# Kernel tuning notes

Measured on AMD Instinct MI355X. Metric: run time of the kernel, lower is better.

The kernel has to match this reference:

```python
import jax, jax.numpy as jnp
import numpy as np

# Config (matches init_kwargs)
B, DIM = 16, 768
HEADS, DHEAD = 12, 64
H_MEM, W_MEM = 16, 16           # memory grid; N = 256 tokens
MAX_AH, MAX_AW = 3, 3
N = H_MEM * W_MEM


def _area_pool(t):
    """t: [B', N, D] laid out on an H_MEM x W_MEM grid.
    Returns (area_sums [B', M, D], area_sizes [M]) over all rectangle sizes
    (ah, aw) with 1<=ah<=MAX_AH, 1<=aw<=MAX_AW, at every valid position,
    via a 2D integral image (summed-area table)."""
    Bp, _, D = t.shape
    g = t.reshape(Bp, H_MEM, W_MEM, D)
    I = jnp.cumsum(jnp.cumsum(g, axis=1), axis=2)
    I = jnp.pad(I, ((0, 0), (1, 0), (1, 0), (0, 0)))  # [B', H+1, W+1, D]
    sums, sizes = [], []
    for ah in range(1, MAX_AH + 1):
        for aw in range(1, MAX_AW + 1):
            s = (I[:, ah:, aw:] - I[:, :-ah, aw:]
                 - I[:, ah:, :-aw] + I[:, :-ah, :-aw])  # [B', H-ah+1, W-aw+1, D]
            n_pos = s.shape[1] * s.shape[2]
            sums.append(s.reshape(Bp, n_pos, D))
            sizes.append(np.full((n_pos,), float(ah * aw), dtype=np.float32))
    return jnp.concatenate(sums, axis=1), jnp.asarray(np.concatenate(sizes))


def setup_inputs() -> dict:
    key = jax.random.key(0)
    ks = jax.random.split(key, 10)
    s = 0.02
    d = dict(
        x=jax.random.normal(ks[0], (B, N, DIM), jnp.float32),
        # to_qkv: Linear(dim, 3*dim, bias=False); stored as (in, out)
        w_qkv=jax.random.normal(ks[1], (DIM, 3 * DIM), jnp.float32) * s,
        # per-head q/k/v projections (dim -> heads*dim_head) with bias
        w_q=jax.random.normal(ks[2], (DIM, HEADS * DHEAD), jnp.float32) * s,
        b_q=jnp.zeros((HEADS * DHEAD,), jnp.float32),
        w_k=jax.random.normal(ks[3], (DIM, HEADS * DHEAD), jnp.float32) * s,
        b_k=jnp.zeros((HEADS * DHEAD,), jnp.float32),
        w_v=jax.random.normal(ks[4], (DIM, HEADS * DHEAD), jnp.float32) * s,
        b_v=jnp.zeros((HEADS * DHEAD,), jnp.float32),
        # output projection (heads*dim_head -> dim)
        w_o=jax.random.normal(ks[5], (HEADS * DHEAD, DIM), jnp.float32) * s,
        b_o=jnp.zeros((DIM,), jnp.float32),
    )
    return d


def reference(x, w_qkv, w_q, b_q, w_k, b_k, w_v, b_v, w_o, b_o):
    # QKV projection + split: 'b n (qkv d) -> qkv b n d'
    qkv = x @ w_qkv                               # [B, N, 3*DIM]
    q, k, v = jnp.split(qkv, 3, axis=-1)          # each [B, N, DIM]

    def to_heads(t, w, b):                        # 'b n (h d) -> (b h) n d'
        return ((t @ w + b)
                .reshape(B, N, HEADS, DHEAD)
                .transpose(0, 2, 1, 3)
                .reshape(B * HEADS, N, DHEAD))

    qh = to_heads(q, w_q, b_q)
    kh = to_heads(k, w_k, b_k)
    vh = to_heads(v, w_v, b_v)

    # Area keys: mean over each area; area values: sum over each area.
    k_sum, sizes = _area_pool(kh)                 # [BH, M, d], [M]
    k_area = k_sum / sizes[None, :, None]
    v_area, _ = _area_pool(vh)                    # [BH, M, d]

    logits = jnp.einsum('bqd,bmd->bqm', qh, k_area)   # [BH, N, M]
    weights = jax.nn.softmax(logits, axis=-1)
    out = jnp.einsum('bqm,bmd->bqd', weights, v_area)  # [BH, N, d]

    # '(b h) n d -> b n (h d)' then output projection
    out = (out.reshape(B, HEADS, N, DHEAD)
              .transpose(0, 2, 1, 3)
              .reshape(B, N, HEADS * DHEAD))
    return out @ w_o + b_o
```

## Files before the change

### kernel.cpp

```cpp
#include <hip/hip_runtime.h>
#include <hip/hip_bf16.h>

typedef __hip_bfloat16 bf16;
typedef __attribute__((ext_vector_type(8))) short short8b;
typedef __attribute__((ext_vector_type(4))) short short4b;
typedef __attribute__((ext_vector_type(4))) float f32x4;

#define NAREA 2025
#define NAREA_PAD 2048

static __device__ __forceinline__ float b2f(bf16 x) { return __bfloat162float(x); }
static __device__ __forceinline__ short f2bs(float f) {
  bf16 h = __float2bfloat16(f);
  return *(short*)&h;
}

__global__ __launch_bounds__(256) void k_cast(
    const float* __restrict__ x, const float* __restrict__ wqkv,
    bf16* __restrict__ xb, bf16* __restrict__ wqkvb)
{
  int idx = (blockIdx.x * 256 + threadIdx.x) * 4;
  const int NX = 4096 * 768;
  float4 v;
  bf16* d;
  if (idx < NX) { v = *(const float4*)(x + idx); d = xb + idx; }
  else { v = *(const float4*)(wqkv + (idx - NX)); d = wqkvb + (idx - NX); }
  short4b s = {f2bs(v.x), f2bs(v.y), f2bs(v.z), f2bs(v.w)};
  *(short4b*)d = s;
}

__global__ __launch_bounds__(256) void k_tcast(
    const float* __restrict__ s0, const float* __restrict__ s1,
    const float* __restrict__ s2, bf16* __restrict__ d0,
    bf16* __restrict__ d1, bf16* __restrict__ d2)
{
  __shared__ float tile[32][33];
  int z = blockIdx.z;
  const float* src = (z == 0) ? s0 : (z == 1) ? s1 : s2;
  bf16* dst = (z == 0) ? d0 : (z == 1) ? d1 : d2;
  int r0 = blockIdx.y * 32, c0 = blockIdx.x * 32;
  int lx = threadIdx.x & 31, ly = threadIdx.x >> 5;
#pragma unroll
  for (int yy = 0; yy < 4; ++yy)
    tile[ly + yy * 8][lx] = src[(size_t)(r0 + ly + yy * 8) * 768 + c0 + lx];
  __syncthreads();
#pragma unroll
  for (int yy = 0; yy < 4; ++yy)
    dst[(size_t)(c0 + ly + yy * 8) * 768 + r0 + lx] =
        __float2bfloat16(tile[lx][ly + yy * 8]);
}


__global__ __launch_bounds__(256) void k_combine_m(
    const bf16* __restrict__ wqkvb, const bf16* __restrict__ wqT,
    const bf16* __restrict__ wkT, const bf16* __restrict__ wvT,
    bf16* __restrict__ WcTb)
{
  __shared__ __align__(16) short As[2][128 * 32];
  __shared__ __align__(16) short Bs[2][128 * 32];
  const int t3 = blockIdx.z;
  const bf16* BT = (t3 == 0) ? wqT : (t3 == 1) ? wkT : wvT;
  const int m0 = blockIdx.y * 128, n0 = blockIdx.x * 128;
  const int tid = threadIdx.x, lane = tid & 63, w = tid >> 6;
  const int tt = lane & 15, q4 = lane >> 4;
  const int moff = (w & 1) * 64, noff = (w >> 1) * 64;
  const int r_a = tid >> 2, kc = (tid & 3) * 8;

  f32x4 acc[4][4];
#pragma unroll
  for (int i = 0; i < 4; ++i)
#pragma unroll
    for (int j = 0; j < 4; ++j) acc[i][j] = (f32x4){0.f, 0.f, 0.f, 0.f};

  uint4 ra0 = *(const uint4*)(wqkvb + (size_t)(m0 + r_a) * 2304 + t3 * 768 + kc);
  uint4 ra1 = *(const uint4*)(wqkvb + (size_t)(m0 + r_a + 64) * 2304 + t3 * 768 + kc);
  uint4 rb0 = *(const uint4*)(BT + (size_t)(n0 + r_a) * 768 + kc);
  uint4 rb1 = *(const uint4*)(BT + (size_t)(n0 + r_a + 64) * 768 + kc);

  for (int it = 0; it < 24; ++it) {
    short* as = As[it & 1];
    short* bs = Bs[it & 1];
    *(uint4*)&as[r_a * 32 + kc] = ra0;
    *(uint4*)&as[(r_a + 64) * 32 + kc] = ra1;
    *(uint4*)&bs[r_a * 32 + kc] = rb0;
    *(uint4*)&bs[(r_a + 64) * 32 + kc] = rb1;
    if (it < 23) {
      int k0 = (it + 1) * 32;
      ra0 = *(const uint4*)(wqkvb + (size_t)(m0 + r_a) * 2304 + t3 * 768 + k0 + kc);
      ra1 = *(const uint4*)(wqkvb + (size_t)(m0 + r_a + 64) * 2304 + t3 * 768 + k0 + kc);
      rb0 = *(const uint4*)(BT + (size_t)(n0 + r_a) * 768 + k0 + kc);
      rb1 = *(const uint4*)(BT + (size_t)(n0 + r_a + 64) * 768 + k0 + kc);
    }
    __syncthreads();
    short8b afr[4], bfr[4];
#pragma unroll
    for (int mt = 0; mt < 4; ++mt)
      afr[mt] = *(const short8b*)&as[(moff + mt * 16 + tt) * 32 + q4 * 8];
#pragma unroll
    for (int nt = 0; nt < 4; ++nt)
      bfr[nt] = *(const short8b*)&bs[(noff + nt * 16 + tt) * 32 + q4 * 8];
#pragma unroll
    for (int mt = 0; mt < 4; ++mt)
#pragma unroll
      for (int nt = 0; nt < 4; ++nt)
        acc[mt][nt] = __builtin_amdgcn_mfma_f32_16x16x32_bf16(afr[mt], bfr[nt], acc[mt][nt], 0, 0, 0);
  }

  bf16* C = WcTb + (size_t)t3 * 768 * 768;
#pragma unroll
  for (int nt = 0; nt < 4; ++nt) {
    int n = n0 + noff + nt * 16 + tt;
#pragma unroll
    for (int mt = 0; mt < 4; ++mt) {
      int mb = m0 + moff + mt * 16 + q4 * 4;
      short4b v = {f2bs(acc[mt][nt][0]), f2bs(acc[mt][nt][1]),
                   f2bs(acc[mt][nt][2]), f2bs(acc[mt][nt][3])};
      *(short4b*)&C[(size_t)n * 768 + mb] = v;
    }
  }
}

__global__ __launch_bounds__(256) void k_proj_m(
    const bf16* __restrict__ xb, const bf16* __restrict__ WcTb,
    const float* __restrict__ bq, const float* __restrict__ bk,
    const float* __restrict__ bv,
    bf16* __restrict__ qh, bf16* __restrict__ kh, bf16* __restrict__ vh)
{
  __shared__ __align__(16) short As[2][128 * 32];
  __shared__ __align__(16) short Bs[2][128 * 32];
  const int t3 = blockIdx.z;
  const bf16* BT = WcTb + (size_t)t3 * 768 * 768;
  const float* bias = (t3 == 0) ? bq : (t3 == 1) ? bk : bv;
  bf16* dst = (t3 == 0) ? qh : (t3 == 1) ? kh : vh;
  const int m0 = blockIdx.y * 128, n0 = blockIdx.x * 128;
  const int tid = threadIdx.x, lane = tid & 63, w = tid >> 6;
  const int tt = lane & 15, q4 = lane >> 4;
  const int moff = (w & 1) * 64, noff = (w >> 1) * 64;
  const int r_a = tid >> 2, kc = (tid & 3) * 8;

  f32x4 acc[4][4];
#pragma unroll
  for (int i = 0; i < 4; ++i)
#pragma unroll
    for (int j = 0; j < 4; ++j) acc[i][j] = (f32x4){0.f, 0.f, 0.f, 0.f};

  uint4 ra0 = *(const uint4*)(xb + (size_t)(m0 + r_a) * 768 + kc);
  uint4 ra1 = *(const uint4*)(xb + (size_t)(m0 + r_a + 64) * 768 + kc);
  uint4 rb0 = *(const uint4*)(BT + (size_t)(n0 + r_a) * 768 + kc);
  uint4 rb1 = *(const uint4*)(BT + (size_t)(n0 + r_a + 64) * 768 + kc);

  for (int it = 0; it < 24; ++it) {
    short* as = As[it & 1];
    short* bs = Bs[it & 1];
    *(uint4*)&as[r_a * 32 + kc] = ra0;
    *(uint4*)&as[(r_a + 64) * 32 + kc] = ra1;
    *(uint4*)&bs[r_a * 32 + kc] = rb0;
    *(uint4*)&bs[(r_a + 64) * 32 + kc] = rb1;
    if (it < 23) {
      int k0 = (it + 1) * 32;
      ra0 = *(const uint4*)(xb + (size_t)(m0 + r_a) * 768 + k0 + kc);
      ra1 = *(const uint4*)(xb + (size_t)(m0 + r_a + 64) * 768 + k0 + kc);
      rb0 = *(const uint4*)(BT + (size_t)(n0 + r_a) * 768 + k0 + kc);
      rb1 = *(const uint4*)(BT + (size_t)(n0 + r_a + 64) * 768 + k0 + kc);
    }
    __syncthreads();
    short8b afr[4], bfr[4];
#pragma unroll
    for (int mt = 0; mt < 4; ++mt)
      afr[mt] = *(const short8b*)&as[(moff + mt * 16 + tt) * 32 + q4 * 8];
#pragma unroll
    for (int nt = 0; nt < 4; ++nt)
      bfr[nt] = *(const short8b*)&bs[(noff + nt * 16 + tt) * 32 + q4 * 8];
#pragma unroll
    for (int mt = 0; mt < 4; ++mt)
#pragma unroll
      for (int nt = 0; nt < 4; ++nt)
        acc[mt][nt] = __builtin_amdgcn_mfma_f32_16x16x32_bf16(afr[mt], bfr[nt], acc[mt][nt], 0, 0, 0);
  }

#pragma unroll
  for (int nt = 0; nt < 4; ++nt) {
    int c = n0 + noff + nt * 16 + tt;
    float bv = bias[c];
    int h = c >> 6, d = c & 63;
#pragma unroll
    for (int mt = 0; mt < 4; ++mt) {
#pragma unroll
      for (int r = 0; r < 4; ++r) {
        int m = m0 + moff + mt * 16 + q4 * 4 + r;
        dst[(((size_t)((m >> 8) * 12 + h)) << 14) + ((m & 255) << 6) + d] =
            __float2bfloat16(acc[mt][nt][r] + bv);
      }
    }
  }
}

__global__ __launch_bounds__(256) void k_out_m(
    const bf16* __restrict__ attno, const bf16* __restrict__ woT,
    const float* __restrict__ bo, float* __restrict__ out)
{
  __shared__ __align__(16) short As[2][128 * 32];
  __shared__ __align__(16) short Bs[2][128 * 32];
  const int m0 = blockIdx.y * 128, n0 = blockIdx.x * 128;
  const int tid = threadIdx.x, lane = tid & 63, w = tid >> 6;
  const int tt = lane & 15, q4 = lane >> 4;
  const int moff = (w & 1) * 64, noff = (w >> 1) * 64;
  const int r_a = tid >> 2, kc = (tid & 3) * 8;

  f32x4 acc[4][4];
#pragma unroll
  for (int i = 0; i < 4; ++i)
#pragma unroll
    for (int j = 0; j < 4; ++j) acc[i][j] = (f32x4){0.f, 0.f, 0.f, 0.f};

  int m_a0 = m0 + r_a, m_a1 = m0 + r_a + 64;
  uint4 ra0 = *(const uint4*)(attno + (((size_t)((m_a0 >> 8) * 12 + (kc >> 6))) << 14) + ((m_a0 & 255) << 6) + (kc & 63));
  uint4 ra1 = *(const uint4*)(attno + (((size_t)((m_a1 >> 8) * 12 + (kc >> 6))) << 14) + ((m_a1 & 255) << 6) + (kc & 63));
  uint4 rb0 = *(const uint4*)(woT + (size_t)(n0 + r_a) * 768 + kc);
  uint4 rb1 = *(const uint4*)(woT + (size_t)(n0 + r_a + 64) * 768 + kc);

  for (int it = 0; it < 24; ++it) {
    short* as = As[it & 1];
    short* bs = Bs[it & 1];
    *(uint4*)&as[r_a * 32 + kc] = ra0;
    *(uint4*)&as[(r_a + 64) * 32 + kc] = ra1;
    *(uint4*)&bs[r_a * 32 + kc] = rb0;
    *(uint4*)&bs[(r_a + 64) * 32 + kc] = rb1;
    if (it < 23) {
      int k = (it + 1) * 32 + kc;
      ra0 = *(const uint4*)(attno + (((size_t)((m_a0 >> 8) * 12 + (k >> 6))) << 14) + ((m_a0 & 255) << 6) + (k & 63));
      ra1 = *(const uint4*)(attno + (((size_t)((m_a1 >> 8) * 12 + (k >> 6))) << 14) + ((m_a1 & 255) << 6) + (k & 63));
      rb0 = *(const uint4*)(woT + (size_t)(n0 + r_a) * 768 + k);
      rb1 = *(const uint4*)(woT + (size_t)(n0 + r_a + 64) * 768 + k);
    }
    __syncthreads();
    short8b afr[4], bfr[4];
#pragma unroll
    for (int mt = 0; mt < 4; ++mt)
      afr[mt] = *(const short8b*)&as[(moff + mt * 16 + tt) * 32 + q4 * 8];
#pragma unroll
    for (int nt = 0; nt < 4; ++nt)
      bfr[nt] = *(const short8b*)&bs[(noff + nt * 16 + tt) * 32 + q4 * 8];
#pragma unroll
    for (int mt = 0; mt < 4; ++mt)
#pragma unroll
      for (int nt = 0; nt < 4; ++nt)
        acc[mt][nt] = __builtin_amdgcn_mfma_f32_16x16x32_bf16(afr[mt], bfr[nt], acc[mt][nt], 0, 0, 0);
  }

#pragma unroll
  for (int nt = 0; nt < 4; ++nt) {
    int c = n0 + noff + nt * 16 + tt;
    float bv = bo[c];
#pragma unroll
    for (int mt = 0; mt < 4; ++mt)
#pragma unroll
      for (int r = 0; r < 4; ++r) {
        int m = m0 + moff + mt * 16 + q4 * 4 + r;
        out[(size_t)m * 768 + c] = acc[mt][nt][r] + bv;
      }
  }
}

__global__ __launch_bounds__(256) void k_rect(int4* __restrict__ rectG,
                                              float* __restrict__ invG)
{
  int m = blockIdx.x * 256 + threadIdx.x;
  if (m >= NAREA_PAD) return;
  int4 rc = make_int4(0, 0, 0, 0);
  float iv = 0.f;
  if (m < NAREA) {
    int rem = m, ah = 1, aw = 1, found = 0;
    for (int a = 1; a <= 3 && !found; ++a)
      for (int w = 1; w <= 3 && !found; ++w) {
        int np = (17 - a) * (17 - w);
        if (rem < np) { ah = a; aw = w; found = 1; }
        else rem -= np;
      }
    int cw = 17 - aw;
    int y = rem / cw, x = rem - y * cw;
    rc.x = (y * 17 + x) * 64;
    rc.y = (y * 17 + (x + aw)) * 64;
    rc.z = ((y + ah) * 17 + x) * 64;
    rc.w = ((y + ah) * 17 + (x + aw)) * 64;
    iv = 1.0f / (float)(ah * aw);
  }
  rectG[m] = rc;
  invG[m] = iv;
}

__global__ __launch_bounds__(128) void k_integral(
    const bf16* __restrict__ kh, const bf16* __restrict__ vh,
    float* __restrict__ Ik, float* __restrict__ Iv)
{
  int bh = blockIdx.x;
  int d = threadIdx.x & 63;
  bool isv = threadIdx.x >= 64;
  const bf16* src = (isv ? vh : kh) + ((size_t)bh << 14);
  float* dst = (isv ? Iv : Ik) + (size_t)bh * 18496;
  float prev[17];
#pragma unroll
  for (int i = 0; i < 17; ++i) prev[i] = 0.f;
#pragma unroll
  for (int xx = 0; xx < 17; ++xx) dst[xx * 64 + d] = 0.f;
#pragma unroll 1
  for (int y = 1; y <= 16; ++y) {
    dst[(y * 17) * 64 + d] = 0.f;
    float rs = 0.f;
#pragma unroll
    for (int xx = 1; xx <= 16; ++xx) {
      rs += b2f(src[((y - 1) * 16 + (xx - 1)) * 64 + d]);
      float cur = prev[xx] + rs;
      dst[(y * 17 + xx) * 64 + d] = cur;
      prev[xx] = cur;
    }
  }
}

__global__ __launch_bounds__(1024) void k_attn_m(
    const bf16* __restrict__ qh, const float* __restrict__ Ik,
    const float* __restrict__ Iv, const int4* __restrict__ rectG,
    const float* __restrict__ invG, bf16* __restrict__ attno)
{
  __shared__ __align__(16) short aK2[2][64 * 72];
  __shared__ __align__(16) short aVt2[2][64 * 72];
  __shared__ __align__(16) short Pb[16][16 * 72];

  const int tid = threadIdx.x;
  const int lane = tid & 63;
  const int w = tid >> 6;
  const int t = lane & 15;
  const int q4 = lane >> 4;
  const int bh = blockIdx.x;

  const float* Ikb = Ik + (size_t)bh * 18496;
  const float* Ivb = Iv + (size_t)bh * 18496;
  const bf16* qbase = qh + ((size_t)bh << 14);

  short8b qf0 = *(const short8b*)(qbase + (w * 16 + t) * 64 + q4 * 8);
  short8b qf1 = *(const short8b*)(qbase + (w * 16 + t) * 64 + 32 + q4 * 8);

  f32x4 O[4];
#pragma unroll
  for (int i = 0; i < 4; ++i) O[i] = (f32x4){0.f, 0.f, 0.f, 0.f};
  float l = 0.f;

  {
    short* aK = aK2[0];
    short* aVt = aVt2[0];
#pragma unroll
    for (int i = 0; i < 4; ++i) {
      int j = w * 4 + i;
      int4 rc = rectG[j];
      float iv = invG[j];
      float kc = Ikb[rc.w + lane] - Ikb[rc.y + lane] - Ikb[rc.z + lane] + Ikb[rc.x + lane];
      float vc = Ivb[rc.w + lane] - Ivb[rc.y + lane] - Ivb[rc.z + lane] + Ivb[rc.x + lane];
      aK[j * 72 + lane] = f2bs(kc * iv);
      aVt[lane * 72 + j] = f2bs(vc);
    }
  }

  for (int it = 0; it < 32; ++it) {
    __syncthreads();
    const short* aK = aK2[it & 1];
    const short* aVt = aVt2[it & 1];
    if (it + 1 < 32) {
      int t0n = (it + 1) * 64;
      short* aKn = aK2[(it + 1) & 1];
      short* aVtn = aVt2[(it + 1) & 1];
#pragma unroll
      for (int i = 0; i < 4; ++i) {
        int j = w * 4 + i;
        int4 rc = rectG[t0n + j];
        float iv = invG[t0n + j];
        float kc = Ikb[rc.w + lane] - Ikb[rc.y + lane] - Ikb[rc.z + lane] + Ikb[rc.x + lane];
        float vc = Ivb[rc.w + lane] - Ivb[rc.y + lane] - Ivb[rc.z + lane] + Ivb[rc.x + lane];
        aKn[j * 72 + lane] = f2bs(kc * iv);
        aVtn[lane * 72 + j] = f2bs(vc);
      }
    }

    const int t0 = it * 64;
    const bool edge = (t0 + 64 > NAREA);
#pragma unroll
    for (int at = 0; at < 4; ++at) {
      short8b af0 = *(const short8b*)&aK[(at * 16 + t) * 72 + q4 * 8];
      short8b af1 = *(const short8b*)&aK[(at * 16 + t) * 72 + 32 + q4 * 8];
      f32x4 s = (f32x4){0.f, 0.f, 0.f, 0.f};
      s = __builtin_amdgcn_mfma_f32_16x16x32_bf16(af0, qf0, s, 0, 0, 0);
      s = __builtin_amdgcn_mfma_f32_16x16x32_bf16(af1, qf1, s, 0, 0, 0);
      float p[4];
#pragma unroll
      for (int r = 0; r < 4; ++r) {
        p[r] = __expf(s[r]);
        if (edge && (t0 + at * 16 + q4 * 4 + r >= NAREA)) p[r] = 0.f;
      }
      l += (p[0] + p[1]) + (p[2] + p[3]);
      short4b pk = (short4b){f2bs(p[0]), f2bs(p[1]), f2bs(p[2]), f2bs(p[3])};
      *(short4b*)&Pb[w][t * 72 + at * 16 + q4 * 4] = pk;
    }
    short8b pf0 = *(const short8b*)&Pb[w][t * 72 + q4 * 8];
    short8b pf1 = *(const short8b*)&Pb[w][t * 72 + 32 + q4 * 8];
#pragma unroll
    for (int nt = 0; nt < 4; ++nt) {
      short8b vf0 = *(const short8b*)&aVt[(nt * 16 + t) * 72 + q4 * 8];
      short8b vf1 = *(const short8b*)&aVt[(nt * 16 + t) * 72 + 32 + q4 * 8];
      O[nt] = __builtin_amdgcn_mfma_f32_16x16x32_bf16(pf0, vf0, O[nt], 0, 0, 0);
      O[nt] = __builtin_amdgcn_mfma_f32_16x16x32_bf16(pf1, vf1, O[nt], 0, 0, 0);
    }
  }

  l += __shfl_xor(l, 16, 64);
  l += __shfl_xor(l, 32, 64);

  bf16* ob = attno + ((size_t)bh << 14);
#pragma unroll
  for (int r = 0; r < 4; ++r) {
    int qrow = q4 * 4 + r;
    float invl = 1.0f / __shfl(l, qrow, 64);
#pragma unroll
    for (int nt = 0; nt < 4; ++nt)
      ob[(w * 16 + qrow) * 64 + nt * 16 + t] = __float2bfloat16(O[nt][r] * invl);
  }
}

extern "C" void kernel_launch(void* const* d_in, const int* in_sizes, int n_in,
                              void* d_out, int out_size, void* d_ws, size_t ws_size,
                              hipStream_t stream) {
  const float* x    = (const float*)d_in[0];
  const float* wqkv = (const float*)d_in[1];
  const float* wq   = (const float*)d_in[2];
  const float* bq   = (const float*)d_in[3];
  const float* wk   = (const float*)d_in[4];
  const float* bk   = (const float*)d_in[5];
  const float* wv   = (const float*)d_in[6];
  const float* bv   = (const float*)d_in[7];
  const float* wo   = (const float*)d_in[8];
  const float* bo   = (const float*)d_in[9];
  float* out = (float*)d_out;

  char* ws = (char*)d_ws;
  char* ob = (char*)d_out;
  const size_t WC_B = 7077888;
  const size_t QH_B = 6291456;

  bf16* xb    = (bf16*)ob;
  bf16* WcTb  = (bf16*)(ob + QH_B);
  bf16* attno = (bf16*)ws;
  int4*  rectG = (int4*)(ws + QH_B);
  float* invG  = (float*)(ws + QH_B + 32768);
  bf16* qh = (bf16*)(ws + WC_B);
  bf16* kh = (bf16*)(ws + WC_B + QH_B);
  bf16* vh = (bf16*)(ws + WC_B + 2 * QH_B);
  bf16* wqkvb = (bf16*)(ws + WC_B);
  bf16* wqT   = (bf16*)(ws + WC_B + 3538944);
  bf16* wkT   = (bf16*)(ws + WC_B + 4718592);
  bf16* wvT   = (bf16*)(ws + WC_B + 5898240);
  float* Ik = (float*)(ws + WC_B + 3 * QH_B);
  float* Iv = Ik + 3551232;
  bf16* woT = (bf16*)(ws + WC_B + 3 * QH_B);

  k_cast<<<dim3(4800), 256, 0, stream>>>(x, wqkv, xb, wqkvb);
  k_tcast<<<dim3(24, 24, 3), 256, 0, stream>>>(wq, wk, wv, wqT, wkT, wvT);
  k_combine_m<<<dim3(6, 6, 3), 256, 0, stream>>>(wqkvb, wqT, wkT, wvT, WcTb);
  k_proj_m<<<dim3(6, 32, 3), 256, 0, stream>>>(xb, WcTb, bq, bk, bv, qh, kh, vh);
  k_rect<<<dim3(8), 256, 0, stream>>>(rectG, invG);
  k_integral<<<dim3(192), 128, 0, stream>>>(kh, vh, Ik, Iv);
  k_attn_m<<<dim3(192), 1024, 0, stream>>>(qh, Ik, Iv, rectG, invG, attno);
  k_tcast<<<dim3(24, 24, 1), 256, 0, stream>>>(wo, wo, wo, woT, woT, woT);
  k_out_m<<<dim3(6, 32), 256, 0, stream>>>(attno, woT, bo, out);
}
```

Baseline: 256.0 us.

## Split attention over area chunks across four blocks and merge partials

The area-attention kernel now splits the 2025-area loop into four chunks per (batch, head), so the grid grows from 192 to 768 blocks. The old grid left many CUs idle. Each split writes an unnormalised partial output and a partial softmax denominator to scratch buffers that reuse dead workspace and output memory. A new merge kernel sums the partials and normalises. The transposed V stores into shared memory are also packed into one 4-short vector write. The cost is an extra kernel launch and extra global traffic for the partials. Storing the partials and denominators in bf16 also loses some precision.

New measurement: 293.1 us. 14.5% more time.

```diff
diff --git a/kernel.cpp b/kernel.cpp
--- a/kernel.cpp
+++ b/kernel.cpp
@@ -13,6 +13,9 @@
 static __device__ __forceinline__ short f2bs(float f) {
   bf16 h = __float2bfloat16(f);
   return *(short*)&h;
+}
+static __device__ __forceinline__ float s2f(short s) {
+  return __uint_as_float(((unsigned)(unsigned short)s) << 16);
 }
 
 __global__ __launch_bounds__(256) void k_cast(
@@ -181,7 +184,7 @@
 #pragma unroll
   for (int nt = 0; nt < 4; ++nt) {
     int c = n0 + noff + nt * 16 + tt;
-    float bv = bias[c];
+    float bvv = bias[c];
     int h = c >> 6, d = c & 63;
 #pragma unroll
     for (int mt = 0; mt < 4; ++mt) {
@@ -189,7 +192,7 @@
       for (int r = 0; r < 4; ++r) {
         int m = m0 + moff + mt * 16 + q4 * 4 + r;
         dst[(((size_t)((m >> 8) * 12 + h)) << 14) + ((m & 255) << 6) + d] =
-            __float2bfloat16(acc[mt][nt][r] + bv);
+            __float2bfloat16(acc[mt][nt][r] + bvv);
       }
     }
   }
@@ -251,13 +254,13 @@
 #pragma unroll
   for (int nt = 0; nt < 4; ++nt) {
     int c = n0 + noff + nt * 16 + tt;
-    float bv = bo[c];
+    float bvv = bo[c];
 #pragma unroll
     for (int mt = 0; mt < 4; ++mt)
 #pragma unroll
       for (int r = 0; r < 4; ++r) {
         int m = m0 + moff + mt * 16 + q4 * 4 + r;
-        out[(size_t)m * 768 + c] = acc[mt][nt][r] + bv;
+        out[(size_t)m * 768 + c] = acc[mt][nt][r] + bvv;
       }
   }
 }
@@ -317,10 +320,11 @@
   }
 }
 
-__global__ __launch_bounds__(1024) void k_attn_m(
+__global__ __launch_bounds__(1024, 8) void k_attn_m(
     const bf16* __restrict__ qh, const float* __restrict__ Ik,
     const float* __restrict__ Iv, const int4* __restrict__ rectG,
-    const float* __restrict__ invG, bf16* __restrict__ attno)
+    const float* __restrict__ invG, bf16* __restrict__ opA,
+    bf16* __restrict__ opB, bf16* __restrict__ lp)
 {
   __shared__ __align__(16) short aK2[2][64 * 72];
   __shared__ __align__(16) short aVt2[2][64 * 72];
@@ -331,7 +335,9 @@
   const int w = tid >> 6;
   const int t = lane & 15;
   const int q4 = lane >> 4;
-  const int bh = blockIdx.x;
+  const int bh = blockIdx.x >> 2;
+  const int split = blockIdx.x & 3;
+  const int itBeg = split * 8, itEnd = itBeg + 8;
 
   const float* Ikb = Ik + (size_t)bh * 18496;
   const float* Ivb = Iv + (size_t)bh * 18496;
@@ -346,28 +352,31 @@
   float l = 0.f;
 
   {
-    short* aK = aK2[0];
-    short* aVt = aVt2[0];
+    short* aK = aK2[itBeg & 1];
+    short* aVt = aVt2[itBeg & 1];
+    short vp[4];
 #pragma unroll
     for (int i = 0; i < 4; ++i) {
-      int j = w * 4 + i;
+      int j = itBeg * 64 + w * 4 + i;
       int4 rc = rectG[j];
       float iv = invG[j];
       float kc = Ikb[rc.w + lane] - Ikb[rc.y + lane] - Ikb[rc.z + lane] + Ikb[rc.x + lane];
       float vc = Ivb[rc.w + lane] - Ivb[rc.y + lane] - Ivb[rc.z + lane] + Ivb[rc.x + lane];
-      aK[j * 72 + lane] = f2bs(kc * iv);
-      aVt[lane * 72 + j] = f2bs(vc);
-    }
-  }
-
-  for (int it = 0; it < 32; ++it) {
+      aK[(w * 4 + i) * 72 + lane] = f2bs(kc * iv);
+      vp[i] = f2bs(vc);
+    }
+    *(short4b*)&aVt[lane * 72 + w * 4] = (short4b){vp[0], vp[1], vp[2], vp[3]};
+  }
+
+  for (int it = itBeg; it < itEnd; ++it) {
     __syncthreads();
     const short* aK = aK2[it & 1];
     const short* aVt = aVt2[it & 1];
-    if (it + 1 < 32) {
+    if (it + 1 < itEnd) {
       int t0n = (it + 1) * 64;
       short* aKn = aK2[(it + 1) & 1];
       short* aVtn = aVt2[(it + 1) & 1];
+      short vp[4];
 #pragma unroll
       for (int i = 0; i < 4; ++i) {
         int j = w * 4 + i;
@@ -376,8 +385,9 @@
         float kc = Ikb[rc.w + lane] - Ikb[rc.y + lane] - Ikb[rc.z + lane] + Ikb[rc.x + lane];
         float vc = Ivb[rc.w + lane] - Ivb[rc.y + lane] - Ivb[rc.z + lane] + Ivb[rc.x + lane];
         aKn[j * 72 + lane] = f2bs(kc * iv);
-        aVtn[lane * 72 + j] = f2bs(vc);
+        vp[i] = f2bs(vc);
       }
+      *(short4b*)&aVtn[lane * 72 + w * 4] = (short4b){vp[0], vp[1], vp[2], vp[3]};
     }
 
     const int t0 = it * 64;
@@ -412,16 +422,41 @@
 
   l += __shfl_xor(l, 16, 64);
   l += __shfl_xor(l, 32, 64);
-
-  bf16* ob = attno + ((size_t)bh << 14);
+  if (lane < 16)
+    lp[(size_t)split * 49152 + bh * 256 + w * 16 + lane] = __float2bfloat16(l);
+
+  bf16* ob = ((split < 2) ? opA + (size_t)split * 3145728
+                          : opB + (size_t)(split - 2) * 3145728) +
+             ((size_t)bh << 14);
 #pragma unroll
   for (int r = 0; r < 4; ++r) {
     int qrow = q4 * 4 + r;
-    float invl = 1.0f / __shfl(l, qrow, 64);
 #pragma unroll
     for (int nt = 0; nt < 4; ++nt)
-      ob[(w * 16 + qrow) * 64 + nt * 16 + t] = __float2bfloat16(O[nt][r] * invl);
-  }
+      ob[(w * 16 + qrow) * 64 + nt * 16 + t] = __float2bfloat16(O[nt][r]);
+  }
+}
+
+__global__ __launch_bounds__(256) void k_merge(
+    const bf16* __restrict__ opA, const bf16* __restrict__ opB,
+    const bf16* __restrict__ lp, bf16* __restrict__ attno)
+{
+  int gid = blockIdx.x * 256 + threadIdx.x;
+  int bq = gid >> 4;
+  int d0 = (gid & 15) * 4;
+  size_t off = (size_t)bq * 64 + d0;
+  float a0 = 0.f, a1 = 0.f, a2 = 0.f, a3 = 0.f, l = 0.f;
+#pragma unroll
+  for (int s = 0; s < 4; ++s) {
+    const bf16* op = (s < 2) ? opA + (size_t)s * 3145728
+                             : opB + (size_t)(s - 2) * 3145728;
+    short4b o = *(const short4b*)(op + off);
+    a0 += s2f(o.x); a1 += s2f(o.y); a2 += s2f(o.z); a3 += s2f(o.w);
+    l += b2f(lp[(size_t)s * 49152 + bq]);
+  }
+  float inv = 1.0f / l;
+  short4b r = {f2bs(a0 * inv), f2bs(a1 * inv), f2bs(a2 * inv), f2bs(a3 * inv)};
+  *(short4b*)(attno + off) = r;
 }
 
 extern "C" void kernel_launch(void* const* d_in, const int* in_sizes, int n_in,
@@ -446,12 +481,15 @@
 
   bf16* xb    = (bf16*)ob;
   bf16* WcTb  = (bf16*)(ob + QH_B);
+  bf16* opB   = (bf16*)ob;
   bf16* attno = (bf16*)ws;
   int4*  rectG = (int4*)(ws + QH_B);
   float* invG  = (float*)(ws + QH_B + 32768);
+  bf16*  lp    = (bf16*)(ws + QH_B + 40960);
   bf16* qh = (bf16*)(ws + WC_B);
   bf16* kh = (bf16*)(ws + WC_B + QH_B);
   bf16* vh = (bf16*)(ws + WC_B + 2 * QH_B);
+  bf16* opA = kh;
   bf16* wqkvb = (bf16*)(ws + WC_B);
   bf16* wqT   = (bf16*)(ws + WC_B + 3538944);
   bf16* wkT   = (bf16*)(ws + WC_B + 4718592);
@@ -466,7 +504,8 @@
   k_proj_m<<<dim3(6, 32, 3), 256, 0, stream>>>(xb, WcTb, bq, bk, bv, qh, kh, vh);
   k_rect<<<dim3(8), 256, 0, stream>>>(rectG, invG);
   k_integral<<<dim3(192), 128, 0, stream>>>(kh, vh, Ik, Iv);
-  k_attn_m<<<dim3(192), 1024, 0, stream>>>(qh, Ik, Iv, rectG, invG, attno);
+  k_attn_m<<<dim3(768), 1024, 0, stream>>>(qh, Ik, Iv, rectG, invG, opA, opB, lp);
+  k_merge<<<dim3(3072), 256, 0, stream>>>(opA, opB, lp, attno);
   k_tcast<<<dim3(24, 24, 1), 256, 0, stream>>>(wo, wo, wo, woT, woT, woT);
   k_out_m<<<dim3(6, 32), 256, 0, stream>>>(attno, woT, bo, out);
 }
```
